# Optimization experiments

Measured on AMD Instinct MI355X. Metric: run time of the kernel, lower is better.

## Reference

```python
import jax, jax.numpy as jnp
import numpy as np

B, S, IN, H, NH = 8, 1024, 512, 512, 8
HD = H // NH
EPS = 1e-5

def _ln(x, g, b):
    m = jnp.mean(x, axis=-1, keepdims=True)
    v = jnp.mean((x - m) ** 2, axis=-1, keepdims=True)
    return (x - m) * jax.lax.rsqrt(v + EPS) * g + b

def setup_inputs() -> dict:
    key = jax.random.key(0)
    ks = iter(jax.random.split(key, 32))
    r = lambda shape: jax.random.normal(next(ks), shape, dtype=jnp.float32) * 0.02
    return {
        "x": jax.random.normal(next(ks), (B, S, IN), dtype=jnp.float32),
        "in_proj_w": r((H, IN)), "in_proj_b": jnp.zeros((H,), jnp.float32),
        "attn_qkv_w": r((3 * H, H)), "attn_qkv_b": jnp.zeros((3 * H,), jnp.float32),
        "attn_out_w": r((H, H)), "attn_out_b": jnp.zeros((H,), jnp.float32),
        "ltc_w1": r((H, 2 * H)), "ltc_b1": jnp.zeros((H,), jnp.float32),
        "ltc_w2": r((H, H)), "ltc_b2": jnp.zeros((H,), jnp.float32),
        "time_w": r((H, H)), "time_b": jnp.zeros((H,), jnp.float32),
        "g_w": r((H, H)), "g_b": jnp.zeros((H,), jnp.float32),
        "hn_w": r((H, H)), "hn_b": jnp.zeros((H,), jnp.float32),
        "norm1_g": jnp.ones((H,), jnp.float32), "norm1_b": jnp.zeros((H,), jnp.float32),
        "norm2_g": jnp.ones((H,), jnp.float32), "norm2_b": jnp.zeros((H,), jnp.float32),
        "out_w": r((IN, H)), "out_b": jnp.zeros((IN,), jnp.float32),
    }

def reference(x, in_proj_w, in_proj_b, attn_qkv_w, attn_qkv_b, attn_out_w, attn_out_b,
              ltc_w1, ltc_b1, ltc_w2, ltc_b2, time_w, time_b, g_w, g_b, hn_w, hn_b,
              norm1_g, norm1_b, norm2_g, norm2_b, out_w, out_b):
    b, s, _ = x.shape
    # input projection
    h = x @ in_proj_w.T + in_proj_b                      # [B,S,H]
    # multi-head self-attention (no mask, eval: no dropout)
    qkv = h @ attn_qkv_w.T + attn_qkv_b                  # [B,S,3H]
    q, k, v = jnp.split(qkv, 3, axis=-1)
    q = q.reshape(b, s, NH, HD)
    k = k.reshape(b, s, NH, HD)
    v = v.reshape(b, s, NH, HD)
    scores = jnp.einsum("bqhd,bkhd->bhqk", q, k) / jnp.sqrt(jnp.float32(HD))
    attn = jax.nn.softmax(scores, axis=-1)
    ctx = jnp.einsum("bhqk,bkhd->bqhd", attn, v).reshape(b, s, H)
    h_att = ctx @ attn_out_w.T + attn_out_b
    h_att = _ln(h + h_att, norm1_g, norm1_b)             # [B,S,H]
    # LTC recurrence over time via scan
    times = jnp.arange(s, dtype=jnp.float32)             # default times, same per batch
    def step(state, inp):
        xt, tt = inp                                      # [B,H], scalar
        combined = jnp.concatenate([xt, state], axis=-1)  # [B,2H]
        feats = jnp.tanh(combined @ ltc_w1.T + ltc_b1) @ ltc_w2.T + ltc_b2
        f_t = jax.nn.sigmoid(feats @ time_w.T + time_b)
        g_x = feats @ g_w.T + g_b
        h_x = feats @ hn_w.T + hn_b
        gate = jax.nn.sigmoid(-f_t * tt)
        h_new = gate * g_x + (1.0 - gate) * h_x
        return h_new, h_new
    init = jnp.zeros((b, H), x.dtype)
    _, outs = jax.lax.scan(step, init, (h_att.transpose(1, 0, 2), times))
    outs = outs.transpose(1, 0, 2)                        # [B,S,H]
    outs = _ln(outs + h_att, norm2_g, norm2_b)
    return outs @ out_w.T + out_b                         # [B,S,IN]
```

## Files before the change

kernel.cpp:

```cpp
#include <hip/hip_runtime.h>
#include <math.h>

#define HALF _Float16
typedef _Float16 half8 __attribute__((ext_vector_type(8)));
typedef float floatx4 __attribute__((ext_vector_type(4)));

#define SPIN_MAX (1 << 20)

__global__ __launch_bounds__(256) void k_cast(const float* __restrict__ s, HALF* __restrict__ d, int n) {
    int i = blockIdx.x * 256 + threadIdx.x;
    if (i < n) d[i] = (HALF)s[i];
}

__global__ __launch_bounds__(256) void k_cast_slice(const float* __restrict__ s, HALF* __restrict__ d, int off) {
    int i = blockIdx.x * 256 + threadIdx.x;
    int r = i >> 9, c = i & 511;
    d[i] = (HALF)s[r * 1024 + off + c];
}

__global__ __launch_bounds__(256) void k_transpose_cast(const float* __restrict__ s, HALF* __restrict__ d) {
    int i = blockIdx.x * 256 + threadIdx.x;
    int r = i >> 9, c = i & 511;
    d[c * 512 + r] = (HALF)s[i];
}

__global__ __launch_bounds__(256) void k_fuse_bias(const float* __restrict__ b2,
    const float* __restrict__ tw, const float* __restrict__ tb,
    const float* __restrict__ gw, const float* __restrict__ gb,
    const float* __restrict__ hw, const float* __restrict__ hb,
    float* __restrict__ bcat) {
    int i = blockIdx.x * 256 + threadIdx.x;
    if (i >= 1536) return;
    int j = i >> 9, n = i & 511;
    const float* W  = (j == 0) ? tw : (j == 1 ? gw : hw);
    const float* bb = (j == 0) ? tb : (j == 1 ? gb : hb);
    float s = bb[n];
    for (int k = 0; k < 512; ++k) s += b2[k] * W[n * 512 + k];
    bcat[i] = s;
}

__global__ __launch_bounds__(256) void k_reorderA(const float* __restrict__ in, float* __restrict__ out) {
    int i = blockIdx.x * 256 + threadIdx.x;
    int nl = i & 7, m = (i >> 3) & 7, blk = (i >> 6) & 63, t = i >> 12;
    out[i] = in[((long long)(m << 10 | t)) * 512 + blk * 8 + nl];
}

__global__ __launch_bounds__(256)
void k_gemm(const HALF* __restrict__ A, int lda, long long sAz,
            const HALF* __restrict__ Bw, int ldb, long long sBz,
            float* __restrict__ Cf, HALF* __restrict__ Ch, int ldc, long long sCz,
            const float* __restrict__ bias, float alpha,
            int M, int N, int K)
{
    __shared__ HALF As[64][72];
    __shared__ HALF Ws[64][72];
    const int tid = threadIdx.x;
    const int bx = blockIdx.x, by = blockIdx.y, z = blockIdx.z;
    A  += (long long)z * sAz;
    Bw += (long long)z * sBz;
    const long long coff = (long long)z * sCz;
    const int wave = tid >> 6, lane = tid & 63;
    const int wrow = (wave >> 1) * 32, wcol = (wave & 1) * 32;
    const int frow = lane & 15, fquad = lane >> 4;
    const int srow = tid >> 3, sch = (tid & 7) * 8;
    floatx4 acc[2][2] = {};
    for (int k0 = 0; k0 < K; k0 += 64) {
        uint4 a0 = *(const uint4*)(A + (long long)(by * 64 + srow) * lda + k0 + sch);
        uint4 a1 = *(const uint4*)(A + (long long)(by * 64 + srow + 32) * lda + k0 + sch);
        uint4 b0 = *(const uint4*)(Bw + (long long)(bx * 64 + srow) * ldb + k0 + sch);
        uint4 b1 = *(const uint4*)(Bw + (long long)(bx * 64 + srow + 32) * ldb + k0 + sch);
        *(uint4*)&As[srow][sch] = a0;
        *(uint4*)&As[srow + 32][sch] = a1;
        *(uint4*)&Ws[srow][sch] = b0;
        *(uint4*)&Ws[srow + 32][sch] = b1;
        __syncthreads();
        #pragma unroll
        for (int ks = 0; ks < 64; ks += 32) {
            half8 fa0 = *(const half8*)&As[wrow + frow][ks + fquad * 8];
            half8 fa1 = *(const half8*)&As[wrow + 16 + frow][ks + fquad * 8];
            half8 fb0 = *(const half8*)&Ws[wcol + frow][ks + fquad * 8];
            half8 fb1 = *(const half8*)&Ws[wcol + 16 + frow][ks + fquad * 8];
            acc[0][0] = __builtin_amdgcn_mfma_f32_16x16x32_f16(fa0, fb0, acc[0][0], 0, 0, 0);
            acc[0][1] = __builtin_amdgcn_mfma_f32_16x16x32_f16(fa0, fb1, acc[0][1], 0, 0, 0);
            acc[1][0] = __builtin_amdgcn_mfma_f32_16x16x32_f16(fa1, fb0, acc[1][0], 0, 0, 0);
            acc[1][1] = __builtin_amdgcn_mfma_f32_16x16x32_f16(fa1, fb1, acc[1][1], 0, 0, 0);
        }
        __syncthreads();
    }
    const int crow = (lane >> 4) * 4, ccol = lane & 15;
    #pragma unroll
    for (int i = 0; i < 2; ++i)
        #pragma unroll
        for (int j = 0; j < 2; ++j) {
            int gn = bx * 64 + wcol + j * 16 + ccol;
            float bv = bias ? bias[gn] : 0.0f;
            #pragma unroll
            for (int r = 0; r < 4; ++r) {
                int gm = by * 64 + wrow + i * 16 + crow + r;
                float v = acc[i][j][r] * alpha + bv;
                long long idx = coff + (long long)gm * ldc + gn;
                if (Cf) Cf[idx] = v;
                if (Ch) Ch[idx] = (HALF)v;
            }
        }
}

__global__ __launch_bounds__(256) void k_qkv_split(const HALF* __restrict__ qkv,
    HALF* __restrict__ Q, HALF* __restrict__ Kt, HALF* __restrict__ VT) {
    long long i = (long long)blockIdx.x * 256 + threadIdx.x;
    int c = (int)(i & 511);
    long long sg = i >> 9;
    int b = (int)(sg >> 10), s = (int)(sg & 1023);
    int h = c >> 6, d = c & 63;
    const HALF* src = qkv + sg * 1536;
    long long bh = (long long)(b * 8 + h);
    long long qi = (bh * 1024 + s) * 64 + d;
    Q[qi]  = src[c];
    Kt[qi] = src[512 + c];
    VT[(bh * 64 + d) * 1024 + s] = src[1024 + c];
}

__global__ __launch_bounds__(256) void k_softmax(HALF* __restrict__ P) {
    long long row = (long long)blockIdx.x * 4 + (threadIdx.x >> 6);
    int lane = threadIdx.x & 63;
    uint4* p = (uint4*)(P + row * 1024);
    union { uint4 u; HALF h[8]; } u0, u1;
    u0.u = p[lane * 2]; u1.u = p[lane * 2 + 1];
    float f[16];
    #pragma unroll
    for (int i = 0; i < 8; ++i) { f[i] = (float)u0.h[i]; f[8 + i] = (float)u1.h[i]; }
    float mx = f[0];
    #pragma unroll
    for (int i = 1; i < 16; ++i) mx = fmaxf(mx, f[i]);
    #pragma unroll
    for (int o = 32; o > 0; o >>= 1) mx = fmaxf(mx, __shfl_xor(mx, o, 64));
    float sm = 0.f;
    #pragma unroll
    for (int i = 0; i < 16; ++i) { f[i] = __expf(f[i] - mx); sm += f[i]; }
    #pragma unroll
    for (int o = 32; o > 0; o >>= 1) sm += __shfl_xor(sm, o, 64);
    float r = 1.0f / sm;
    #pragma unroll
    for (int i = 0; i < 8; ++i) { u0.h[i] = (HALF)(f[i] * r); u1.h[i] = (HALF)(f[8 + i] * r); }
    p[lane * 2] = u0.u; p[lane * 2 + 1] = u1.u;
}

__global__ __launch_bounds__(256) void k_ln_add(const float* __restrict__ X, const float* __restrict__ Y,
    const float* __restrict__ g, const float* __restrict__ bb,
    float* __restrict__ o32, HALF* __restrict__ o16) {
    long long row = (long long)blockIdx.x * 4 + (threadIdx.x >> 6);
    int lane = threadIdx.x & 63;
    const float4* xp = (const float4*)(X + row * 512);
    const float4* yp = (const float4*)(Y + row * 512);
    float v[8];
    float s = 0.f, s2 = 0.f;
    #pragma unroll
    for (int i = 0; i < 2; ++i) {
        float4 a = xp[lane * 2 + i], c = yp[lane * 2 + i];
        float t0 = a.x + c.x, t1 = a.y + c.y, t2 = a.z + c.z, t3 = a.w + c.w;
        v[i * 4 + 0] = t0; v[i * 4 + 1] = t1; v[i * 4 + 2] = t2; v[i * 4 + 3] = t3;
        s += t0 + t1 + t2 + t3;
        s2 += t0 * t0 + t1 * t1 + t2 * t2 + t3 * t3;
    }
    #pragma unroll
    for (int o = 32; o > 0; o >>= 1) { s += __shfl_xor(s, o, 64); s2 += __shfl_xor(s2, o, 64); }
    float mean = s * (1.0f / 512.0f);
    float var = s2 * (1.0f / 512.0f) - mean * mean;
    float rstd = rsqrtf(var + 1e-5f);
    #pragma unroll
    for (int i = 0; i < 8; ++i) {
        int c = lane * 8 + i;
        float o = (v[i] - mean) * rstd * g[c] + bb[c];
        if (o32) o32[row * 512 + c] = o;
        if (o16) o16[row * 512 + c] = (HALF)o;
    }
}

__device__ __forceinline__ floatx4 mfma16(half8 a, half8 b, floatx4 c) {
    return __builtin_amdgcn_mfma_f32_16x16x32_f16(a, b, c, 0, 0, 0);
}
__device__ __forceinline__ unsigned long long pack4h(float a, float b, float c, float d) {
    union { unsigned short u; HALF h; } x0, x1, x2, x3;
    x0.h = (HALF)a; x1.h = (HALF)b; x2.h = (HALF)c; x3.h = (HALF)d;
    return (unsigned long long)x0.u | ((unsigned long long)x1.u << 16)
         | ((unsigned long long)x2.u << 32) | ((unsigned long long)x3.u << 48);
}

__global__ __launch_bounds__(256, 1)
void k_ltc_scan(const float* __restrict__ AscanR, const HALF* __restrict__ W1hg,
                const HALF* __restrict__ Wcatg, const float* __restrict__ bcat,
                HALF* __restrict__ Sbuf, HALF* __restrict__ Tbuf,
                float* __restrict__ outs, int* __restrict__ flags)
{
    __shared__ unsigned long long SL[1088];
    const int tid = threadIdx.x;
    const int wv = tid >> 6, lane = tid & 63;
    const int blk = blockIdx.x * 4 + wv;
    const int n0 = blk * 8;
    const int c = lane & 15, q = lane >> 4;
    const int nW = n0 + (c & 7);
    const int kq = q * 8;
    const bool valid = (q < 2) && (c < 8);
    int* flag1 = flags;
    int* flag2 = flags + 32;
    unsigned long long* Su = (unsigned long long*)Sbuf;
    unsigned long long* Tu = (unsigned long long*)Tbuf;
    const int pidx = blk * 16 + c * 2 + q;
    const char* SLb = (const char*)SL;

    half8 aW1[16];
    half8 aWc[3][16];
    #pragma unroll
    for (int kb = 0; kb < 16; ++kb)
        aW1[kb] = *(const half8*)(W1hg + (long long)nW * 512 + kb * 32 + kq);
    #pragma unroll
    for (int j = 0; j < 3; ++j)
        #pragma unroll
        for (int kb = 0; kb < 16; ++kb)
            aWc[j][kb] = *(const half8*)(Wcatg + ((long long)j * 512 + nW) * 512 + kb * 32 + kq);
    floatx4 binit[3];
    #pragma unroll
    for (int j = 0; j < 3; ++j) {
        float4 bv = *(const float4*)(bcat + j * 512 + n0 + (q & 1) * 4);
        binit[j][0] = bv.x; binit[j][1] = bv.y; binit[j][2] = bv.z; binit[j][3] = bv.w;
    }

    for (int t = 0; t < 1024; ++t) {
        float4 aval = *(const float4*)(AscanR + (long long)t * 4096 + blk * 64 + (c & 7) * 8 + (q & 1) * 4);

        if (wv == 0) {
            int spin = 0;
            while (true) {
                int v = __hip_atomic_load(&flag2[lane & 15], __ATOMIC_RELAXED, __HIP_MEMORY_SCOPE_SYSTEM);
                if (__ballot(v >= t) == ~0ull) break;
                __builtin_amdgcn_s_sleep(1);
                if (++spin > SPIN_MAX) break;
            }
        }
        __syncthreads();
        {
            const int i0 = tid * 4;
            unsigned long long a0 = __hip_atomic_load(Su + i0,     __ATOMIC_RELAXED, __HIP_MEMORY_SCOPE_SYSTEM);
            unsigned long long a1 = __hip_atomic_load(Su + i0 + 1, __ATOMIC_RELAXED, __HIP_MEMORY_SCOPE_SYSTEM);
            unsigned long long a2 = __hip_atomic_load(Su + i0 + 2, __ATOMIC_RELAXED, __HIP_MEMORY_SCOPE_SYSTEM);
            unsigned long long a3 = __hip_atomic_load(Su + i0 + 3, __ATOMIC_RELAXED, __HIP_MEMORY_SCOPE_SYSTEM);
            SL[i0] = a0; SL[i0 + 1] = a1; SL[i0 + 2] = a2; SL[i0 + 3] = a3;
        }
        __syncthreads();
        floatx4 c1a = {0.f, 0.f, 0.f, 0.f}, c1b = {0.f, 0.f, 0.f, 0.f};
        #pragma unroll
        for (int kb = 0; kb < 16; kb += 2) {
            half8 b0 = *(const half8*)(SLb + kb * 512 + q * 128 + c * 16);
            half8 b1 = *(const half8*)(SLb + (kb + 1) * 512 + q * 128 + c * 16);
            c1a = mfma16(aW1[kb],     b0, c1a);
            c1b = mfma16(aW1[kb + 1], b1, c1b);
        }
        floatx4 c1 = c1a + c1b;
        float tv0 = tanhf(c1[0] + aval.x);
        float tv1 = tanhf(c1[1] + aval.y);
        float tv2 = tanhf(c1[2] + aval.z);
        float tv3 = tanhf(c1[3] + aval.w);
        if (valid)
            __hip_atomic_store(Tu + pidx, pack4h(tv0, tv1, tv2, tv3),
                               __ATOMIC_RELAXED, __HIP_MEMORY_SCOPE_SYSTEM);
        asm volatile("s_waitcnt vmcnt(0)" ::: "memory");
        __syncthreads();
        if (tid == 0)
            __hip_atomic_store(&flag1[blockIdx.x], t + 1, __ATOMIC_RELAXED, __HIP_MEMORY_SCOPE_SYSTEM);

        if (wv == 0) {
            int spin = 0;
            while (true) {
                int v = __hip_atomic_load(&flag1[lane & 15], __ATOMIC_RELAXED, __HIP_MEMORY_SCOPE_SYSTEM);
                if (__ballot(v >= t + 1) == ~0ull) break;
                __builtin_amdgcn_s_sleep(1);
                if (++spin > SPIN_MAX) break;
            }
        }
        __syncthreads();
        {
            const int i0 = tid * 4;
            unsigned long long a0 = __hip_atomic_load(Tu + i0,     __ATOMIC_RELAXED, __HIP_MEMORY_SCOPE_SYSTEM);
            unsigned long long a1 = __hip_atomic_load(Tu + i0 + 1, __ATOMIC_RELAXED, __HIP_MEMORY_SCOPE_SYSTEM);
            unsigned long long a2 = __hip_atomic_load(Tu + i0 + 2, __ATOMIC_RELAXED, __HIP_MEMORY_SCOPE_SYSTEM);
            unsigned long long a3 = __hip_atomic_load(Tu + i0 + 3, __ATOMIC_RELAXED, __HIP_MEMORY_SCOPE_SYSTEM);
            SL[i0] = a0; SL[i0 + 1] = a1; SL[i0 + 2] = a2; SL[i0 + 3] = a3;
        }
        __syncthreads();
        floatx4 c2_0 = binit[0], c2_1 = binit[1], c2_2 = binit[2];
        #pragma unroll
        for (int kb = 0; kb < 16; ++kb) {
            half8 bT = *(const half8*)(SLb + kb * 512 + q * 128 + c * 16);
            c2_0 = mfma16(aWc[0][kb], bT, c2_0);
            c2_1 = mfma16(aWc[1][kb], bT, c2_1);
            c2_2 = mfma16(aWc[2][kb], bT, c2_2);
        }
        float sn[4];
        const float tf = (float)t;
        #pragma unroll
        for (int r = 0; r < 4; ++r) {
            float f = 1.0f / (1.0f + __expf(-c2_0[r]));
            float gate = 1.0f / (1.0f + __expf(f * tf));
            sn[r] = gate * c2_1[r] + (1.0f - gate) * c2_2[r];
        }
        if (valid)
            __hip_atomic_store(Su + pidx, pack4h(sn[0], sn[1], sn[2], sn[3]),
                               __ATOMIC_RELAXED, __HIP_MEMORY_SCOPE_SYSTEM);
        asm volatile("s_waitcnt vmcnt(0)" ::: "memory");
        __syncthreads();
        if (tid == 0)
            __hip_atomic_store(&flag2[blockIdx.x], t + 1, __ATOMIC_RELAXED, __HIP_MEMORY_SCOPE_SYSTEM);
        if (valid) {
            float4 ov; ov.x = sn[0]; ov.y = sn[1]; ov.z = sn[2]; ov.w = sn[3];
            *(float4*)(outs + ((long long)(c << 10 | t)) * 512 + n0 + q * 4) = ov;
        }
    }
}

extern "C" void kernel_launch(void* const* d_in, const int* in_sizes, int n_in,
                              void* d_out, int out_size, void* d_ws, size_t ws_size,
                              hipStream_t stream) {
    (void)in_sizes; (void)n_in; (void)out_size; (void)ws_size;
    const float* x       = (const float*)d_in[0];
    const float* w_in_f  = (const float*)d_in[1];
    const float* b_in    = (const float*)d_in[2];
    const float* w_qkv_f = (const float*)d_in[3];
    const float* b_qkv   = (const float*)d_in[4];
    const float* w_ao_f  = (const float*)d_in[5];
    const float* b_ao    = (const float*)d_in[6];
    const float* w1_f    = (const float*)d_in[7];
    const float* b1      = (const float*)d_in[8];
    const float* w2_f    = (const float*)d_in[9];
    const float* b2      = (const float*)d_in[10];
    const float* tw_f    = (const float*)d_in[11];
    const float* tb      = (const float*)d_in[12];
    const float* gw_f    = (const float*)d_in[13];
    const float* gb      = (const float*)d_in[14];
    const float* hw_f    = (const float*)d_in[15];
    const float* hb      = (const float*)d_in[16];
    const float* n1g     = (const float*)d_in[17];
    const float* n1b     = (const float*)d_in[18];
    const float* n2g     = (const float*)d_in[19];
    const float* n2b     = (const float*)d_in[20];
    const float* w_out_f = (const float*)d_in[21];
    const float* b_out   = (const float*)d_in[22];
    float* out = (float*)d_out;

    char* p = (char*)d_ws;
    auto alloc = [&](size_t n) { char* r = p; p += (n + 255) & ~(size_t)255; return r; };
    HALF* w_in   = (HALF*)alloc(512 * 512 * 2);
    HALF* w_qkv  = (HALF*)alloc(1536 * 512 * 2);
    HALF* w_ao   = (HALF*)alloc(512 * 512 * 2);
    HALF* w_out  = (HALF*)alloc(512 * 512 * 2);
    HALF* w_time = (HALF*)alloc(512 * 512 * 2);
    HALF* w_g    = (HALF*)alloc(512 * 512 * 2);
    HALF* w_hn   = (HALF*)alloc(512 * 512 * 2);
    HALF* W2T    = (HALF*)alloc(512 * 512 * 2);
    HALF* W1x    = (HALF*)alloc(512 * 512 * 2);
    HALF* W1h    = (HALF*)alloc(512 * 512 * 2);
    HALF* Wcat   = (HALF*)alloc(3 * 512 * 512 * 2);
    float* bcat  = (float*)alloc(3 * 512 * 4 + 64);
    HALF* xb     = (HALF*)alloc(8192ll * 512 * 2);
    float* h32   = (float*)alloc(8192ll * 512 * 4);
    HALF* h16    = (HALF*)alloc(8192ll * 512 * 2);
    HALF* qkv16  = (HALF*)alloc(8192ll * 1536 * 2);
    HALF* Q16    = (HALF*)alloc(8192ll * 512 * 2);
    HALF* K16    = (HALF*)alloc(8192ll * 512 * 2);
    HALF* VT16   = (HALF*)alloc(8192ll * 512 * 2);
    HALF* P16    = (HALF*)alloc(8ll * 1024 * 1024 * 2);
    HALF* Sbuf   = (HALF*)alloc(8192 + 256);
    HALF* Tbuf   = (HALF*)alloc(8192 + 256);
    int*  flags  = (int*)alloc(512);

    HALF*  ctx16      = xb;
    float* attnproj32 = (float*)qkv16;
    float* hatt32     = (float*)P16;
    HALF*  hatt16     = VT16;
    float* Ascan32    = h32;
    float* AscanR     = (float*)K16;
    float* outs32     = (float*)qkv16;
    HALF*  y16        = h16;

    hipMemsetAsync(Sbuf, 0, (8192 + 256) + (8192 + 256) + 512, stream);

    k_cast<<<1024, 256, 0, stream>>>(w_in_f, w_in, 262144);
    k_cast<<<3072, 256, 0, stream>>>(w_qkv_f, w_qkv, 786432);
    k_cast<<<1024, 256, 0, stream>>>(w_ao_f, w_ao, 262144);
    k_cast<<<1024, 256, 0, stream>>>(w_out_f, w_out, 262144);
    k_cast<<<1024, 256, 0, stream>>>(tw_f, w_time, 262144);
    k_cast<<<1024, 256, 0, stream>>>(gw_f, w_g, 262144);
    k_cast<<<1024, 256, 0, stream>>>(hw_f, w_hn, 262144);
    k_cast<<<16384, 256, 0, stream>>>(x, xb, 4194304);
    k_transpose_cast<<<1024, 256, 0, stream>>>(w2_f, W2T);
    k_cast_slice<<<1024, 256, 0, stream>>>(w1_f, W1x, 0);
    k_cast_slice<<<1024, 256, 0, stream>>>(w1_f, W1h, 512);
    k_fuse_bias<<<6, 256, 0, stream>>>(b2, tw_f, tb, gw_f, gb, hw_f, hb, bcat);

    dim3 g88(8, 8, 1);
    k_gemm<<<g88, 256, 0, stream>>>(w_time, 512, 0, W2T, 512, 0, nullptr, Wcat,          512, 0, nullptr, 1.0f, 512, 512, 512);
    k_gemm<<<g88, 256, 0, stream>>>(w_g,    512, 0, W2T, 512, 0, nullptr, Wcat + 262144, 512, 0, nullptr, 1.0f, 512, 512, 512);
    k_gemm<<<g88, 256, 0, stream>>>(w_hn,   512, 0, W2T, 512, 0, nullptr, Wcat + 524288, 512, 0, nullptr, 1.0f, 512, 512, 512);

    dim3 gh(8, 128, 1);
    k_gemm<<<gh, 256, 0, stream>>>(xb, 512, 0, w_in, 512, 0, h32, h16, 512, 0, b_in, 1.0f, 8192, 512, 512);
    dim3 gq(24, 128, 1);
    k_gemm<<<gq, 256, 0, stream>>>(h16, 512, 0, w_qkv, 512, 0, nullptr, qkv16, 1536, 0, b_qkv, 1.0f, 8192, 1536, 512);
    k_qkv_split<<<16384, 256, 0, stream>>>(qkv16, Q16, K16, VT16);

    for (int c = 0; c < 8; ++c) {
        dim3 gs(16, 16, 8);
        k_gemm<<<gs, 256, 0, stream>>>(Q16 + c * 524288, 64, 65536, K16 + c * 524288, 64, 65536,
                                       nullptr, P16, 1024, 1048576, nullptr, 0.125f, 1024, 1024, 64);
        k_softmax<<<2048, 256, 0, stream>>>(P16);
        dim3 gc(1, 16, 8);
        k_gemm<<<gc, 256, 0, stream>>>(P16, 1024, 1048576, VT16 + c * 524288, 1024, 65536,
                                       nullptr, ctx16 + (long long)c * 524288, 512, 64, nullptr, 1.0f, 1024, 64, 1024);
    }

    k_gemm<<<gh, 256, 0, stream>>>(ctx16, 512, 0, w_ao, 512, 0, attnproj32, nullptr, 512, 0, b_ao, 1.0f, 8192, 512, 512);
    k_ln_add<<<2048, 256, 0, stream>>>(h32, attnproj32, n1g, n1b, hatt32, hatt16);

    k_gemm<<<gh, 256, 0, stream>>>(hatt16, 512, 0, W1x, 512, 0, Ascan32, nullptr, 512, 0, b1, 1.0f, 8192, 512, 512);
    k_reorderA<<<16384, 256, 0, stream>>>(Ascan32, AscanR);

    k_ltc_scan<<<16, 256, 0, stream>>>(AscanR, W1h, Wcat, bcat, Sbuf, Tbuf, outs32, flags);

    k_ln_add<<<2048, 256, 0, stream>>>(outs32, hatt32, n2g, n2b, nullptr, y16);
    k_gemm<<<gh, 256, 0, stream>>>(y16, 512, 0, w_out, 512, 0, out, nullptr, 512, 0, b_out, 1.0f, 8192, 512, 512);
}
```

Measured before the change: 6.189 ms.

## Replace flag-based inter-block sync with tagged data words in LTC scan

The recurrent scan kernel no longer publishes per-block flags after a vmcnt wait and barrier. Each 64-bit store now carries two fp16 values plus a 16-bit step tag. Readers poll the data words directly until every tag matches the expected step, then use the payload. This removes a flag round-trip and store drain from each of the two cross-block exchanges per timestep. In exchange the exchanged data doubles in size, and correctness now rests on 64-bit store atomicity and on the tag not wrapping.

```diff
diff --git a/kernel.cpp b/kernel.cpp
--- a/kernel.cpp
+++ b/kernel.cpp
@@ -5,7 +5,7 @@
 typedef _Float16 half8 __attribute__((ext_vector_type(8)));
 typedef float floatx4 __attribute__((ext_vector_type(4)));
 
-#define SPIN_MAX (1 << 20)
+#define SPIN_MAX (1 << 16)
 
 __global__ __launch_bounds__(256) void k_cast(const float* __restrict__ s, HALF* __restrict__ d, int n) {
     int i = blockIdx.x * 256 + threadIdx.x;
@@ -179,20 +179,21 @@
 __device__ __forceinline__ floatx4 mfma16(half8 a, half8 b, floatx4 c) {
     return __builtin_amdgcn_mfma_f32_16x16x32_f16(a, b, c, 0, 0, 0);
 }
-__device__ __forceinline__ unsigned long long pack4h(float a, float b, float c, float d) {
-    union { unsigned short u; HALF h; } x0, x1, x2, x3;
-    x0.h = (HALF)a; x1.h = (HALF)b; x2.h = (HALF)c; x3.h = (HALF)d;
+__device__ __forceinline__ unsigned long long pack2h_tag(float a, float b, unsigned tag) {
+    union { unsigned short u; HALF h; } x0, x1;
+    x0.h = (HALF)a; x1.h = (HALF)b;
     return (unsigned long long)x0.u | ((unsigned long long)x1.u << 16)
-         | ((unsigned long long)x2.u << 32) | ((unsigned long long)x3.u << 48);
+         | ((unsigned long long)tag << 48);
 }
 
 __global__ __launch_bounds__(256, 1)
 void k_ltc_scan(const float* __restrict__ AscanR, const HALF* __restrict__ W1hg,
                 const HALF* __restrict__ Wcatg, const float* __restrict__ bcat,
-                HALF* __restrict__ Sbuf, HALF* __restrict__ Tbuf,
-                float* __restrict__ outs, int* __restrict__ flags)
+                unsigned long long* __restrict__ Sbuf, unsigned long long* __restrict__ Tbuf,
+                float* __restrict__ outs)
 {
-    __shared__ unsigned long long SL[1088];
+    __shared__ unsigned int SLu[2176];
+    __shared__ int s_ok[2];
     const int tid = threadIdx.x;
     const int wv = tid >> 6, lane = tid & 63;
     const int blk = blockIdx.x * 4 + wv;
@@ -201,12 +202,11 @@
     const int nW = n0 + (c & 7);
     const int kq = q * 8;
     const bool valid = (q < 2) && (c < 8);
-    int* flag1 = flags;
-    int* flag2 = flags + 32;
-    unsigned long long* Su = (unsigned long long*)Sbuf;
-    unsigned long long* Tu = (unsigned long long*)Tbuf;
     const int pidx = blk * 16 + c * 2 + q;
-    const char* SLb = (const char*)SL;
+    const int i0 = tid * 8;
+    const char* SLb = (const char*)SLu;
+
+    if (tid < 2) s_ok[tid] = 1;
 
     half8 aW1[16];
     half8 aWc[3][16];
@@ -225,28 +225,35 @@
         binit[j][0] = bv.x; binit[j][1] = bv.y; binit[j][2] = bv.z; binit[j][3] = bv.w;
     }
 
+    auto stage_wait = [&](const unsigned long long* __restrict__ P, unsigned tag) {
+        int spin = 0;
+        int pp = 0;
+        for (;;) {
+            unsigned long long v[8];
+            #pragma unroll
+            for (int k = 0; k < 8; ++k)
+                v[k] = __hip_atomic_load(P + i0 + k, __ATOMIC_RELAXED, __HIP_MEMORY_SCOPE_SYSTEM);
+            __syncthreads();
+            if (tid == 0) s_ok[pp ^ 1] = 1;
+            int ok = 1;
+            #pragma unroll
+            for (int k = 0; k < 8; ++k) {
+                ok &= ((unsigned)(v[k] >> 48) == tag);
+                SLu[i0 + k] = (unsigned)v[k];
+            }
+            if (!ok) s_ok[pp] = 0;
+            __syncthreads();
+            if (s_ok[pp]) return;
+            pp ^= 1;
+            if (++spin > SPIN_MAX) return;
+        }
+    };
+
     for (int t = 0; t < 1024; ++t) {
         float4 aval = *(const float4*)(AscanR + (long long)t * 4096 + blk * 64 + (c & 7) * 8 + (q & 1) * 4);
 
-        if (wv == 0) {
-            int spin = 0;
-            while (true) {
-                int v = __hip_atomic_load(&flag2[lane & 15], __ATOMIC_RELAXED, __HIP_MEMORY_SCOPE_SYSTEM);
-                if (__ballot(v >= t) == ~0ull) break;
-                __builtin_amdgcn_s_sleep(1);
-                if (++spin > SPIN_MAX) break;
-            }
-        }
-        __syncthreads();
-        {
-            const int i0 = tid * 4;
-            unsigned long long a0 = __hip_atomic_load(Su + i0,     __ATOMIC_RELAXED, __HIP_MEMORY_SCOPE_SYSTEM);
-            unsigned long long a1 = __hip_atomic_load(Su + i0 + 1, __ATOMIC_RELAXED, __HIP_MEMORY_SCOPE_SYSTEM);
-            unsigned long long a2 = __hip_atomic_load(Su + i0 + 2, __ATOMIC_RELAXED, __HIP_MEMORY_SCOPE_SYSTEM);
-            unsigned long long a3 = __hip_atomic_load(Su + i0 + 3, __ATOMIC_RELAXED, __HIP_MEMORY_SCOPE_SYSTEM);
-            SL[i0] = a0; SL[i0 + 1] = a1; SL[i0 + 2] = a2; SL[i0 + 3] = a3;
-        }
-        __syncthreads();
+        stage_wait(Sbuf, (unsigned)t);
+
         floatx4 c1a = {0.f, 0.f, 0.f, 0.f}, c1b = {0.f, 0.f, 0.f, 0.f};
         #pragma unroll
         for (int kb = 0; kb < 16; kb += 2) {
@@ -260,33 +267,15 @@
         float tv1 = tanhf(c1[1] + aval.y);
         float tv2 = tanhf(c1[2] + aval.z);
         float tv3 = tanhf(c1[3] + aval.w);
-        if (valid)
-            __hip_atomic_store(Tu + pidx, pack4h(tv0, tv1, tv2, tv3),
+        if (valid) {
+            __hip_atomic_store(Tbuf + pidx * 2,     pack2h_tag(tv0, tv1, (unsigned)(t + 1)),
                                __ATOMIC_RELAXED, __HIP_MEMORY_SCOPE_SYSTEM);
-        asm volatile("s_waitcnt vmcnt(0)" ::: "memory");
-        __syncthreads();
-        if (tid == 0)
-            __hip_atomic_store(&flag1[blockIdx.x], t + 1, __ATOMIC_RELAXED, __HIP_MEMORY_SCOPE_SYSTEM);
-
-        if (wv == 0) {
-            int spin = 0;
-            while (true) {
-                int v = __hip_atomic_load(&flag1[lane & 15], __ATOMIC_RELAXED, __HIP_MEMORY_SCOPE_SYSTEM);
-                if (__ballot(v >= t + 1) == ~0ull) break;
-                __builtin_amdgcn_s_sleep(1);
-                if (++spin > SPIN_MAX) break;
-            }
-        }
-        __syncthreads();
-        {
-            const int i0 = tid * 4;
-            unsigned long long a0 = __hip_atomic_load(Tu + i0,     __ATOMIC_RELAXED, __HIP_MEMORY_SCOPE_SYSTEM);
-            unsigned long long a1 = __hip_atomic_load(Tu + i0 + 1, __ATOMIC_RELAXED, __HIP_MEMORY_SCOPE_SYSTEM);
-            unsigned long long a2 = __hip_atomic_load(Tu + i0 + 2, __ATOMIC_RELAXED, __HIP_MEMORY_SCOPE_SYSTEM);
-            unsigned long long a3 = __hip_atomic_load(Tu + i0 + 3, __ATOMIC_RELAXED, __HIP_MEMORY_SCOPE_SYSTEM);
-            SL[i0] = a0; SL[i0 + 1] = a1; SL[i0 + 2] = a2; SL[i0 + 3] = a3;
-        }
-        __syncthreads();
+            __hip_atomic_store(Tbuf + pidx * 2 + 1, pack2h_tag(tv2, tv3, (unsigned)(t + 1)),
+                               __ATOMIC_RELAXED, __HIP_MEMORY_SCOPE_SYSTEM);
+        }
+
+        stage_wait(Tbuf, (unsigned)(t + 1));
+
         floatx4 c2_0 = binit[0], c2_1 = binit[1], c2_2 = binit[2];
         #pragma unroll
         for (int kb = 0; kb < 16; ++kb) {
@@ -303,13 +292,12 @@
             float gate = 1.0f / (1.0f + __expf(f * tf));
             sn[r] = gate * c2_1[r] + (1.0f - gate) * c2_2[r];
         }
-        if (valid)
-            __hip_atomic_store(Su + pidx, pack4h(sn[0], sn[1], sn[2], sn[3]),
+        if (valid) {
+            __hip_atomic_store(Sbuf + pidx * 2,     pack2h_tag(sn[0], sn[1], (unsigned)(t + 1)),
                                __ATOMIC_RELAXED, __HIP_MEMORY_SCOPE_SYSTEM);
-        asm volatile("s_waitcnt vmcnt(0)" ::: "memory");
-        __syncthreads();
-        if (tid == 0)
-            __hip_atomic_store(&flag2[blockIdx.x], t + 1, __ATOMIC_RELAXED, __HIP_MEMORY_SCOPE_SYSTEM);
+            __hip_atomic_store(Sbuf + pidx * 2 + 1, pack2h_tag(sn[2], sn[3], (unsigned)(t + 1)),
+                               __ATOMIC_RELAXED, __HIP_MEMORY_SCOPE_SYSTEM);
+        }
         if (valid) {
             float4 ov; ov.x = sn[0]; ov.y = sn[1]; ov.z = sn[2]; ov.w = sn[3];
             *(float4*)(outs + ((long long)(c << 10 | t)) * 512 + n0 + q * 4) = ov;
@@ -368,9 +356,8 @@
     HALF* K16    = (HALF*)alloc(8192ll * 512 * 2);
     HALF* VT16   = (HALF*)alloc(8192ll * 512 * 2);
     HALF* P16    = (HALF*)alloc(8ll * 1024 * 1024 * 2);
-    HALF* Sbuf   = (HALF*)alloc(8192 + 256);
-    HALF* Tbuf   = (HALF*)alloc(8192 + 256);
-    int*  flags  = (int*)alloc(512);
+    unsigned long long* Sbuf = (unsigned long long*)alloc(16384 + 256);
+    unsigned long long* Tbuf = (unsigned long long*)alloc(16384 + 256);
 
     HALF*  ctx16      = xb;
     float* attnproj32 = (float*)qkv16;
@@ -381,7 +368,7 @@
     float* outs32     = (float*)qkv16;
     HALF*  y16        = h16;
 
-    hipMemsetAsync(Sbuf, 0, (8192 + 256) + (8192 + 256) + 512, stream);
+    hipMemsetAsync(Sbuf, 0, (16384 + 256) * 2, stream);
 
     k_cast<<<1024, 256, 0, stream>>>(w_in_f, w_in, 262144);
     k_cast<<<3072, 256, 0, stream>>>(w_qkv_f, w_qkv, 786432);
@@ -423,7 +410,7 @@
     k_gemm<<<gh, 256, 0, stream>>>(hatt16, 512, 0, W1x, 512, 0, Ascan32, nullptr, 512, 0, b1, 1.0f, 8192, 512, 512);
     k_reorderA<<<16384, 256, 0, stream>>>(Ascan32, AscanR);
 
-    k_ltc_scan<<<16, 256, 0, stream>>>(AscanR, W1h, Wcat, bcat, Sbuf, Tbuf, outs32, flags);
+    k_ltc_scan<<<16, 256, 0, stream>>>(AscanR, W1h, Wcat, bcat, Sbuf, Tbuf, outs32);
 
     k_ln_add<<<2048, 256, 0, stream>>>(outs32, hatt32, n2g, n2b, nullptr, y16);
     k_gemm<<<gh, 256, 0, stream>>>(y16, 512, 0, w_out, 512, 0, out, nullptr, 512, 0, b_out, 1.0f, 8192, 512, 512);
```

Result: slower. 7.524 ms (+21.6%).
